# Kernel optimization log

Hardware: AMD Instinct MI355X
Metric: run time of the kernel (lower is better)

Reference implementation:

```python
import jax, jax.numpy as jnp
import numpy as np

B, S, IN = 64, 600, 3
H, C, K = 512, 80, 20
U = 64  # char_len
OUT = 1 + 6 * K


def lstm_cell(x, h, c, W_ih, W_hh, b_ih, b_hh):
    # PyTorch LSTMCell: gates order i, f, g, o
    gates = x @ W_ih.T + b_ih + h @ W_hh.T + b_hh
    i, f, g, o = jnp.split(gates, 4, axis=1)
    i = jax.nn.sigmoid(i)
    f = jax.nn.sigmoid(f)
    g = jnp.tanh(g)
    o = jax.nn.sigmoid(o)
    c_new = f * c + i * g
    h_new = o * jnp.tanh(c_new)
    return h_new, c_new


def setup_inputs() -> dict:
    key = jax.random.key(0)
    ks = jax.random.split(key, 16)
    sc = 0.05
    return {
        "x": jax.random.normal(ks[0], (B, S, IN), jnp.float32),
        "chars": jax.random.uniform(ks[1], (B, U, C), jnp.float32),
        "W_ih1": jax.random.normal(ks[2], (4 * H, IN + C), jnp.float32) * sc,
        "W_hh1": jax.random.normal(ks[3], (4 * H, H), jnp.float32) * sc,
        "b_ih1": jnp.zeros((4 * H,), jnp.float32),
        "b_hh1": jnp.zeros((4 * H,), jnp.float32),
        "W_win": jax.random.normal(ks[4], (3 * K, H), jnp.float32) * sc,
        "b_win": jnp.zeros((3 * K,), jnp.float32),
        "W_ih2": jax.random.normal(ks[5], (4 * H, IN + C), jnp.float32) * sc,
        "W_hh2": jax.random.normal(ks[6], (4 * H, H), jnp.float32) * sc,
        "b_ih2": jnp.zeros((4 * H,), jnp.float32),
        "b_hh2": jnp.zeros((4 * H,), jnp.float32),
        "W_mdn": jax.random.normal(ks[7], (OUT, H), jnp.float32) * sc,
        "b_mdn": jnp.zeros((OUT,), jnp.float32),
    }


def reference(x, chars, W_ih1, W_hh1, b_ih1, b_hh1, W_win, b_win,
              W_ih2, W_hh2, b_ih2, b_hh2, W_mdn, b_mdn):
    u = jnp.arange(U, dtype=x.dtype)[None, None, :]  # [1,1,U]

    def step(carry, pt):
        h1, c1, h2, c2, window, kappa_prev = carry
        inp1 = jnp.concatenate([pt, window], axis=1)           # [B, IN+C]
        h1, c1 = lstm_cell(inp1, h1, c1, W_ih1, W_hh1, b_ih1, b_hh1)
        # Gaussian window attention (Graves)
        wout = h1 @ W_win.T + b_win                            # [B, 3K]
        a, b_, k = jnp.split(wout, 3, axis=1)
        alpha = jnp.exp(a)[:, :, None]                         # [B,K,1]
        beta = jnp.exp(b_)[:, :, None]
        kappa = kappa_prev + jnp.exp(k)                        # [B,K]
        phi = jnp.sum(alpha * jnp.exp(-beta * (kappa[:, :, None] - u) ** 2), axis=1)  # [B,U]
        window = jnp.einsum('bu,buc->bc', phi, chars)          # [B,C]
        inp2 = jnp.concatenate([pt, window], axis=1)
        h2, c2 = lstm_cell(inp2, h2, c2, W_ih2, W_hh2, b_ih2, b_hh2)
        return (h1, c1, h2, c2, window, kappa), h2

    z = jnp.zeros((B, H), x.dtype)
    carry0 = (z, z, z, z, jnp.zeros((B, C), x.dtype), jnp.zeros((B, K), x.dtype))
    _, hs2 = jax.lax.scan(step, carry0, jnp.transpose(x, (1, 0, 2)))  # [S,B,H]
    outputs = jnp.transpose(hs2, (1, 0, 2)).reshape(-1, H)             # [B*S,H]
    mdn = outputs @ W_mdn.T + b_mdn                                     # [B*S,OUT]

    eos = jax.nn.sigmoid(mdn[:, 0]).reshape(-1, 1)
    pi, mu1, mu2, sigma1, sigma2, rho = jnp.split(mdn[:, 1:], 6, axis=1)
    pi = jax.nn.softmax(pi, axis=1)
    sigma1 = jnp.exp(sigma1)
    sigma2 = jnp.exp(sigma2)
    rho = jnp.tanh(rho)
    return eos, pi, mu1, mu2, sigma1, sigma2, rho
```

## Files before the change

### kernel.cpp

```cpp
#include <hip/hip_runtime.h>


typedef unsigned int u32;
typedef unsigned short u16;
typedef unsigned long long u64;
typedef short short8 __attribute__((ext_vector_type(8)));
typedef float floatx4 __attribute__((ext_vector_type(4)));
typedef u32 u32x4 __attribute__((ext_vector_type(4)));

#define NBLK   193
#define NGEMM  128
#define AGG_BID 192
#define NTHR   256
#define SLEN   600

#define OFF_FLAG 0ull
#define OFF_GEN  16384ull
#define OFF_H1P  32768ull
#define OFF_H2P  (OFF_H1P + 131072ull)
#define OFF_WP   (OFF_H2P + 131072ull)
#define OFF_XHI  (OFF_WP + 24576ull)
#define OFF_XLO  (OFF_XHI + 2457600ull)
#define OFF_HS2  (OFF_XLO + 2457600ull)
#define WS_NEED  (OFF_HS2 + 39321600ull)

__device__ __forceinline__ float bf2f(short h) {
  return __uint_as_float(((u32)(u16)h) << 16);
}
__device__ __forceinline__ u16 f2bf(float f) {
  u32 u = __float_as_uint(f);
  u += 0x7fffu + ((u >> 16) & 1u);
  return (u16)(u >> 16);
}
__device__ __forceinline__ float fsig(float x) { return 1.0f / (1.0f + __expf(-x)); }
__device__ __forceinline__ float ftanh_(float x) { return 2.0f / (1.0f + __expf(-2.0f * x)) - 1.0f; }

__device__ __forceinline__ float lstm_point(floatx4 g, float& c) {
  float i  = fsig(g[0]);
  float f  = fsig(g[1]);
  float gg = ftanh_(g[2]);
  float o  = fsig(g[3]);
  c = f * c + i * gg;
  return o * ftanh_(c);
}

__device__ __forceinline__ u32 pack_split(float v) {
  u32 b = __float_as_uint(v);
  float rem = v - __uint_as_float(b & 0xffff0000u);
  return (b >> 16) | ((u32)f2bf(rem) << 16);
}

__device__ __forceinline__ void st_coh(u32* p, u32 v) {
  __hip_atomic_store(p, v, __ATOMIC_RELAXED, __HIP_MEMORY_SCOPE_AGENT);
}
__device__ __forceinline__ u32 ld_coh(const u32* p) {
  return __hip_atomic_load((u32*)p, __ATOMIC_RELAXED, __HIP_MEMORY_SCOPE_AGENT);
}

__device__ __forceinline__ void ld_pk8(const u32* p, short8& hi, short8& lo) {
  u64 d0 = __hip_atomic_load((u64*)(p + 0), __ATOMIC_RELAXED, __HIP_MEMORY_SCOPE_AGENT);
  u64 d1 = __hip_atomic_load((u64*)(p + 2), __ATOMIC_RELAXED, __HIP_MEMORY_SCOPE_AGENT);
  u64 d2 = __hip_atomic_load((u64*)(p + 4), __ATOMIC_RELAXED, __HIP_MEMORY_SCOPE_AGENT);
  u64 d3 = __hip_atomic_load((u64*)(p + 6), __ATOMIC_RELAXED, __HIP_MEMORY_SCOPE_AGENT);
  u32 a0 = (u32)d0, a1 = (u32)(d0 >> 32), a2 = (u32)d1, a3 = (u32)(d1 >> 32);
  u32 a4 = (u32)d2, a5 = (u32)(d2 >> 32), a6 = (u32)d3, a7 = (u32)(d3 >> 32);
  u32x4 h, l;
  h[0] = __builtin_amdgcn_perm(a1, a0, 0x05040100u); l[0] = __builtin_amdgcn_perm(a1, a0, 0x07060302u);
  h[1] = __builtin_amdgcn_perm(a3, a2, 0x05040100u); l[1] = __builtin_amdgcn_perm(a3, a2, 0x07060302u);
  h[2] = __builtin_amdgcn_perm(a5, a4, 0x05040100u); l[2] = __builtin_amdgcn_perm(a5, a4, 0x07060302u);
  h[3] = __builtin_amdgcn_perm(a7, a6, 0x05040100u); l[3] = __builtin_amdgcn_perm(a7, a6, 0x07060302u);
  hi = __builtin_bit_cast(short8, h);
  lo = __builtin_bit_cast(short8, l);
}

__device__ __forceinline__ void sync_wait(u32* flags, u32* gen, u32 lgen, int bid) {
  if (bid == AGG_BID) {
    const int i = threadIdx.x;
    if (i < NBLK) {
      u32 sp = 0;
      while (ld_coh(&flags[i * 16]) < lgen) {
        __builtin_amdgcn_s_sleep(1);
        if (++sp > (1u << 22)) break;
      }
    }
    __syncthreads();
    if (threadIdx.x < 8) st_coh(&gen[threadIdx.x * 16], lgen);
  } else {
    if (threadIdx.x == 0) {
      u32 sp = 0;
      while (ld_coh(&gen[(bid & 7) * 16]) < lgen) {
        __builtin_amdgcn_s_sleep(2);
        if (++sp > (1u << 22)) break;
      }
    }
  }
}

__device__ __forceinline__ void sync_light(u32* flags, u32* gen, u32& lgen, int bid) {
  asm volatile("s_waitcnt vmcnt(0) lgkmcnt(0)" ::: "memory");
  __syncthreads();
  lgen++;
  if (threadIdx.x == 0) st_coh(&flags[bid * 16], lgen);
  sync_wait(flags, gen, lgen, bid);
  __syncthreads();
  asm volatile("" ::: "memory");
}

__device__ __forceinline__ void sync_full(u32* flags, u32* gen, u32& lgen, int bid) {
  __syncthreads();
  lgen++;
  if (threadIdx.x == 0) {
    __threadfence();
    st_coh(&flags[bid * 16], lgen);
  }
  sync_wait(flags, gen, lgen, bid);
  if (threadIdx.x == 0) __threadfence();
  __syncthreads();
  asm volatile("" ::: "memory");
}

__global__ void init_ws(unsigned char* ws) {
  const int gtid = blockIdx.x * 256 + threadIdx.x;
  u32* flg = (u32*)(ws + OFF_FLAG);
  for (int i = gtid; i < NBLK * 16; i += 64 * 256) flg[i] = 0u;
  u32* gn = (u32*)(ws + OFF_GEN);
  if (gtid < 128) gn[gtid] = 0u;
  u32* h2p = (u32*)(ws + OFF_H2P);
  for (int i = gtid; i < 64 * 512; i += 64 * 256) h2p[i] = 0u;
  u32* wp = (u32*)(ws + OFF_WP);
  for (int i = gtid; i < 64 * 96; i += 64 * 256) wp[i] = 0u;
}

__global__ __launch_bounds__(NTHR, 1) void rnn_kernel(
    const float* __restrict__ x, const float* __restrict__ chars,
    const float* __restrict__ Wih1, const float* __restrict__ Whh1,
    const float* __restrict__ bih1, const float* __restrict__ bhh1,
    const float* __restrict__ Wwin, const float* __restrict__ bwin,
    const float* __restrict__ Wih2, const float* __restrict__ Whh2,
    const float* __restrict__ bih2, const float* __restrict__ bhh2,
    const float* __restrict__ Wmdn, const float* __restrict__ bmdn,
    float* __restrict__ out, unsigned char* __restrict__ ws)
{
  const int bid = blockIdx.x;
  const int tid = threadIdx.x;
  const int wid = tid >> 6;
  const int lane = tid & 63;

  u32* flags = (u32*)(ws + OFF_FLAG);
  u32* gen   = (u32*)(ws + OFF_GEN);
  u32* h1p   = (u32*)(ws + OFF_H1P);
  u32* h2p   = (u32*)(ws + OFF_H2P);
  u32* wp    = (u32*)(ws + OFF_WP);
  u16* xhi   = (u16*)(ws + OFF_XHI);
  u16* xlo   = (u16*)(ws + OFF_XLO);
  u16* hs2   = (u16*)(ws + OFF_HS2);

  u32 lgen = 0;

  __shared__ __align__(16) u16 hifrag_s[40 * 512];
  __shared__ __align__(16) u16 lofrag_s[40 * 512];
  __shared__ __align__(16) float chars_s[64 * 80];
  __shared__ __align__(16) float smem_f[512];
  __shared__ float wout_s[64];
  __shared__ float al_s[20], be_s[20], kp_s[20];

  for (int i = bid * NTHR + tid; i < SLEN * 64 * 32; i += NBLK * NTHR) {
    int t = i >> 11;
    int r = i & 2047;
    int bb = r >> 5, q = r & 31;
    float v = (q < 3) ? x[((size_t)bb * SLEN + t) * 3 + q] : 0.0f;
    u32 b = __float_as_uint(v);
    xhi[i] = (u16)(b >> 16);
    xlo[i] = f2bf(v - __uint_as_float(b & 0xffff0000u));
  }

  const bool isg = (bid < NGEMM);
  const bool isw = (bid >= NGEMM && bid < NGEMM + 64);

  float bs1[4], bs2[4];
  float c1 = 0.0f, c2 = 0.0f;
  int b_row = 0, hc = 0;
  float bw = 0.0f;
  const int kg = (lane >> 4) * 8;

  if (isg) {
    b_row = 16 * wid + (lane & 15);
    hc = 4 * bid + (lane >> 4);
    if (wid == 0) {
      const int ra = lane & 15;
      const int origA = (ra & 3) * 512 + 4 * bid + (ra >> 2);
      #pragma unroll
      for (int ks = 0; ks < 20; ++ks) {
        short8 v1h, v1l, v2h, v2l;
        #pragma unroll
        for (int j = 0; j < 8; ++j) {
          int k = 32 * ks + kg + j;
          float a1 = 0.0f, a2 = 0.0f;
          if (k < 512) {
            a1 = Whh1[(size_t)origA * 512 + k];
            a2 = Whh2[(size_t)origA * 512 + k];
          } else if (k < 592) {
            a1 = Wih1[(size_t)origA * 83 + 3 + (k - 512)];
            a2 = Wih2[(size_t)origA * 83 + 3 + (k - 512)];
          } else if (k >= 608 && k < 611) {
            a1 = Wih1[(size_t)origA * 83 + (k - 608)];
            a2 = Wih2[(size_t)origA * 83 + (k - 608)];
          }
          u32 b1 = __float_as_uint(a1), b2 = __float_as_uint(a2);
          v1h[j] = (short)(u16)(b1 >> 16);
          v2h[j] = (short)(u16)(b2 >> 16);
          v1l[j] = (short)f2bf(a1 - __uint_as_float(b1 & 0xffff0000u));
          v2l[j] = (short)f2bf(a2 - __uint_as_float(b2 & 0xffff0000u));
        }
        *(short8*)(hifrag_s + ((0 * 20 + ks) << 9) + (lane << 3)) = v1h;
        *(short8*)(hifrag_s + ((1 * 20 + ks) << 9) + (lane << 3)) = v2h;
        *(short8*)(lofrag_s + ((0 * 20 + ks) << 9) + (lane << 3)) = v1l;
        *(short8*)(lofrag_s + ((1 * 20 + ks) << 9) + (lane << 3)) = v2l;
      }
    }
    #pragma unroll
    for (int r = 0; r < 4; ++r) {
      bs1[r] = bih1[r * 512 + hc] + bhh1[r * 512 + hc];
      bs2[r] = bih2[r * 512 + hc] + bhh2[r * 512 + hc];
    }
  } else if (isw) {
    const int b = bid - NGEMM;
    for (int i = tid; i < 64 * 80; i += NTHR)
      chars_s[i] = chars[(size_t)b * 5120 + i];
    if (tid < 20) kp_s[tid] = 0.0f;
    if (tid < 60) bw = bwin[tid];
  }

  sync_full(flags, gen, lgen, bid);

  if (isg) {
    floatx4 a = { bs1[0], bs1[1], bs1[2], bs1[3] };
    floatx4 b = {0.f,0.f,0.f,0.f}, c = {0.f,0.f,0.f,0.f};
    short8 xh = *(const short8*)(xhi + (size_t)b_row * 32 + kg);
    short8 xl = *(const short8*)(xlo + (size_t)b_row * 32 + kg);
    short8 ah = *(const short8*)(hifrag_s + ((0 * 20 + 19) << 9) + (lane << 3));
    short8 al = *(const short8*)(lofrag_s + ((0 * 20 + 19) << 9) + (lane << 3));
    a = __builtin_amdgcn_mfma_f32_16x16x32_bf16(ah, xh, a, 0, 0, 0);
    b = __builtin_amdgcn_mfma_f32_16x16x32_bf16(ah, xl, b, 0, 0, 0);
    c = __builtin_amdgcn_mfma_f32_16x16x32_bf16(al, xh, c, 0, 0, 0);
    float h = lstm_point(a + b + c, c1);
    st_coh(&h1p[b_row * 512 + hc], pack_split(h));
  }

  sync_light(flags, gen, lgen, bid);

  for (int t = 0; t < SLEN; ++t) {
    floatx4 a1a = {0.f,0.f,0.f,0.f}, a1b = a1a, a1c = a1a;
    floatx4 a2a = {0.f,0.f,0.f,0.f}, a2b = a2a, a2c = a2a;

    if (isg) {
      a2a[0] = bs2[0]; a2a[1] = bs2[1]; a2a[2] = bs2[2]; a2a[3] = bs2[3];
      #pragma unroll
      for (int g = 0; g < 2; ++g) {
        short8 bh[8], bl[8];
        #pragma unroll
        for (int k = 0; k < 8; ++k)
          ld_pk8(h2p + b_row * 512 + (g * 8 + k) * 32 + kg, bh[k], bl[k]);
        #pragma unroll
        for (int k = 0; k < 8; ++k) {
          const int ks = g * 8 + k;
          short8 ah = *(const short8*)(hifrag_s + ((20 + ks) << 9) + (lane << 3));
          short8 al = *(const short8*)(lofrag_s + ((20 + ks) << 9) + (lane << 3));
          a2a = __builtin_amdgcn_mfma_f32_16x16x32_bf16(ah, bh[k], a2a, 0, 0, 0);
          a2b = __builtin_amdgcn_mfma_f32_16x16x32_bf16(ah, bl[k], a2b, 0, 0, 0);
          a2c = __builtin_amdgcn_mfma_f32_16x16x32_bf16(al, bh[k], a2c, 0, 0, 0);
        }
      }
      {
        short8 xh = *(const short8*)(xhi + ((size_t)t * 64 + b_row) * 32 + kg);
        short8 xl = *(const short8*)(xlo + ((size_t)t * 64 + b_row) * 32 + kg);
        short8 ah = *(const short8*)(hifrag_s + ((20 + 19) << 9) + (lane << 3));
        short8 al = *(const short8*)(lofrag_s + ((20 + 19) << 9) + (lane << 3));
        a2a = __builtin_amdgcn_mfma_f32_16x16x32_bf16(ah, xh, a2a, 0, 0, 0);
        a2b = __builtin_amdgcn_mfma_f32_16x16x32_bf16(ah, xl, a2b, 0, 0, 0);
        a2c = __builtin_amdgcn_mfma_f32_16x16x32_bf16(al, xh, a2c, 0, 0, 0);
      }
      if (t < SLEN - 1) {
        a1a[0] = bs1[0]; a1a[1] = bs1[1]; a1a[2] = bs1[2]; a1a[3] = bs1[3];
        #pragma unroll
        for (int g = 0; g < 2; ++g) {
          short8 bh[8], bl[8];
          #pragma unroll
          for (int k = 0; k < 8; ++k)
            ld_pk8(h1p + b_row * 512 + (g * 8 + k) * 32 + kg, bh[k], bl[k]);
          #pragma unroll
          for (int k = 0; k < 8; ++k) {
            const int ks = g * 8 + k;
            short8 ah = *(const short8*)(hifrag_s + (ks << 9) + (lane << 3));
            short8 al = *(const short8*)(lofrag_s + (ks << 9) + (lane << 3));
            a1a = __builtin_amdgcn_mfma_f32_16x16x32_bf16(ah, bh[k], a1a, 0, 0, 0);
            a1b = __builtin_amdgcn_mfma_f32_16x16x32_bf16(ah, bl[k], a1b, 0, 0, 0);
            a1c = __builtin_amdgcn_mfma_f32_16x16x32_bf16(al, bh[k], a1c, 0, 0, 0);
          }
        }
        short8 xh = *(const short8*)(xhi + ((size_t)(t + 1) * 64 + b_row) * 32 + kg);
        short8 xl = *(const short8*)(xlo + ((size_t)(t + 1) * 64 + b_row) * 32 + kg);
        short8 ah = *(const short8*)(hifrag_s + (19 << 9) + (lane << 3));
        short8 al = *(const short8*)(lofrag_s + (19 << 9) + (lane << 3));
        a1a = __builtin_amdgcn_mfma_f32_16x16x32_bf16(ah, xh, a1a, 0, 0, 0);
        a1b = __builtin_amdgcn_mfma_f32_16x16x32_bf16(ah, xl, a1b, 0, 0, 0);
        a1c = __builtin_amdgcn_mfma_f32_16x16x32_bf16(al, xh, a1c, 0, 0, 0);
      }
    } else if (isw) {
      const int b = bid - NGEMM;
      for (int k = tid; k < 512; k += NTHR) {
        u32 p = ld_coh(&h1p[b * 512 + k]);
        smem_f[k] = bf2f((short)(u16)p) + bf2f((short)(u16)(p >> 16));
      }
      __syncthreads();
      const int col = tid & 63;
      const int kq  = tid >> 6;
      float p = 0.0f;
      if (col < 60) {
        const floatx4* wr = (const floatx4*)(Wwin + (size_t)col * 512 + kq * 128);
        const floatx4* hr = (const floatx4*)(smem_f + kq * 128);
        #pragma unroll
        for (int k4 = 0; k4 < 32; ++k4) {
          floatx4 wv = wr[k4];
          floatx4 hv = hr[k4];
          p = fmaf(wv[0], hv[0], p);
          p = fmaf(wv[1], hv[1], p);
          p = fmaf(wv[2], hv[2], p);
          p = fmaf(wv[3], hv[3], p);
        }
      }
      __syncthreads();
      smem_f[tid] = p;
      __syncthreads();
      if (tid < 60)
        wout_s[tid] = smem_f[tid] + smem_f[64 + tid] + smem_f[128 + tid] + smem_f[192 + tid] + bw;
      __syncthreads();
      if (tid < 20) {
        al_s[tid] = __expf(wout_s[tid]);
        be_s[tid] = __expf(wout_s[20 + tid]);
        kp_s[tid] += __expf(wout_s[40 + tid]);
      }
      __syncthreads();
      if (tid < 64) {
        float u = (float)tid;
        float ph = 0.0f;
        #pragma unroll
        for (int k = 0; k < 20; ++k) {
          float d = kp_s[k] - u;
          ph = fmaf(al_s[k], __expf(-be_s[k] * d * d), ph);
        }
        smem_f[256 + tid] = ph;
      }
      __syncthreads();
      if (tid < 80) {
        float wv = 0.0f;
        for (int u = 0; u < 64; ++u)
          wv = fmaf(smem_f[256 + u], chars_s[u * 80 + tid], wv);
        st_coh(&wp[b * 96 + tid], pack_split(wv));
      }
    }

    sync_light(flags, gen, lgen, bid);

    if (isg) {
      short8 wh0, wl0, wh1, wl1, wh2, wl2;
      ld_pk8(wp + b_row * 96 +  0 + kg, wh0, wl0);
      ld_pk8(wp + b_row * 96 + 32 + kg, wh1, wl1);
      ld_pk8(wp + b_row * 96 + 64 + kg, wh2, wl2);
      short8 a2h0 = *(const short8*)(hifrag_s + ((20 + 16) << 9) + (lane << 3));
      short8 a2h1 = *(const short8*)(hifrag_s + ((20 + 17) << 9) + (lane << 3));
      short8 a2h2 = *(const short8*)(hifrag_s + ((20 + 18) << 9) + (lane << 3));
      short8 a2l0 = *(const short8*)(lofrag_s + ((20 + 16) << 9) + (lane << 3));
      short8 a2l1 = *(const short8*)(lofrag_s + ((20 + 17) << 9) + (lane << 3));
      short8 a2l2 = *(const short8*)(lofrag_s + ((20 + 18) << 9) + (lane << 3));
      a2a = __builtin_amdgcn_mfma_f32_16x16x32_bf16(a2h0, wh0, a2a, 0, 0, 0);
      a2b = __builtin_amdgcn_mfma_f32_16x16x32_bf16(a2h0, wl0, a2b, 0, 0, 0);
      a2c = __builtin_amdgcn_mfma_f32_16x16x32_bf16(a2l0, wh0, a2c, 0, 0, 0);
      a2a = __builtin_amdgcn_mfma_f32_16x16x32_bf16(a2h1, wh1, a2a, 0, 0, 0);
      a2b = __builtin_amdgcn_mfma_f32_16x16x32_bf16(a2h1, wl1, a2b, 0, 0, 0);
      a2c = __builtin_amdgcn_mfma_f32_16x16x32_bf16(a2l1, wh1, a2c, 0, 0, 0);
      a2a = __builtin_amdgcn_mfma_f32_16x16x32_bf16(a2h2, wh2, a2a, 0, 0, 0);
      a2b = __builtin_amdgcn_mfma_f32_16x16x32_bf16(a2h2, wl2, a2b, 0, 0, 0);
      a2c = __builtin_amdgcn_mfma_f32_16x16x32_bf16(a2l2, wh2, a2c, 0, 0, 0);
      float h2v = lstm_point(a2a + a2b + a2c, c2);
      st_coh(&h2p[b_row * 512 + hc], pack_split(h2v));
      hs2[((size_t)b_row * SLEN + t) * 512 + hc] = f2bf(h2v);
      if (t < SLEN - 1) {
        short8 a1h0 = *(const short8*)(hifrag_s + (16 << 9) + (lane << 3));
        short8 a1h1 = *(const short8*)(hifrag_s + (17 << 9) + (lane << 3));
        short8 a1h2 = *(const short8*)(hifrag_s + (18 << 9) + (lane << 3));
        short8 a1l0 = *(const short8*)(lofrag_s + (16 << 9) + (lane << 3));
        short8 a1l1 = *(const short8*)(lofrag_s + (17 << 9) + (lane << 3));
        short8 a1l2 = *(const short8*)(lofrag_s + (18 << 9) + (lane << 3));
        a1a = __builtin_amdgcn_mfma_f32_16x16x32_bf16(a1h0, wh0, a1a, 0, 0, 0);
        a1b = __builtin_amdgcn_mfma_f32_16x16x32_bf16(a1h0, wl0, a1b, 0, 0, 0);
        a1c = __builtin_amdgcn_mfma_f32_16x16x32_bf16(a1l0, wh0, a1c, 0, 0, 0);
        a1a = __builtin_amdgcn_mfma_f32_16x16x32_bf16(a1h1, wh1, a1a, 0, 0, 0);
        a1b = __builtin_amdgcn_mfma_f32_16x16x32_bf16(a1h1, wl1, a1b, 0, 0, 0);
        a1c = __builtin_amdgcn_mfma_f32_16x16x32_bf16(a1l1, wh1, a1c, 0, 0, 0);
        a1a = __builtin_amdgcn_mfma_f32_16x16x32_bf16(a1h2, wh2, a1a, 0, 0, 0);
        a1b = __builtin_amdgcn_mfma_f32_16x16x32_bf16(a1h2, wl2, a1b, 0, 0, 0);
        a1c = __builtin_amdgcn_mfma_f32_16x16x32_bf16(a1l2, wh2, a1c, 0, 0, 0);
        float h1v = lstm_point(a1a + a1b + a1c, c1);
        st_coh(&h1p[b_row * 512 + hc], pack_split(h1v));
      }
    }

    sync_light(flags, gen, lgen, bid);
  }

  sync_full(flags, gen, lgen, bid);

  {
    const int row = bid * NTHR + tid;
    if (row < 38400) {
      const u16* hrow = hs2 + (size_t)row * 512;
      {
        float acc = bmdn[0];
        for (int k8 = 0; k8 < 512; k8 += 8) {
          short8 hv = *(const short8*)(hrow + k8);
          #pragma unroll
          for (int j = 0; j < 8; ++j) acc = fmaf(bf2f(hv[j]), Wmdn[k8 + j], acc);
        }
        out[row] = fsig(acc);
      }
      {
        float a[20];
        #pragma unroll
        for (int cc = 0; cc < 20; ++cc) a[cc] = bmdn[1 + cc];
        for (int k8 = 0; k8 < 512; k8 += 8) {
          short8 hv = *(const short8*)(hrow + k8);
          float hf[8];
          #pragma unroll
          for (int j = 0; j < 8; ++j) hf[j] = bf2f(hv[j]);
          #pragma unroll
          for (int cc = 0; cc < 20; ++cc) {
            const float* wr = Wmdn + (size_t)(1 + cc) * 512 + k8;
            #pragma unroll
            for (int j = 0; j < 8; ++j) a[cc] = fmaf(hf[j], wr[j], a[cc]);
          }
        }
        float mx = a[0];
        #pragma unroll
        for (int cc = 1; cc < 20; ++cc) mx = fmaxf(mx, a[cc]);
        float s = 0.0f;
        #pragma unroll
        for (int cc = 0; cc < 20; ++cc) { a[cc] = __expf(a[cc] - mx); s += a[cc]; }
        float inv = 1.0f / s;
        float* po = out + 38400 + (size_t)row * 20;
        #pragma unroll
        for (int cc = 0; cc < 20; ++cc) po[cc] = a[cc] * inv;
      }
      for (int grp = 1; grp <= 5; ++grp) {
        float a[20];
        #pragma unroll
        for (int cc = 0; cc < 20; ++cc) a[cc] = bmdn[1 + 20 * grp + cc];
        for (int k8 = 0; k8 < 512; k8 += 8) {
          short8 hv = *(const short8*)(hrow + k8);
          float hf[8];
          #pragma unroll
          for (int j = 0; j < 8; ++j) hf[j] = bf2f(hv[j]);
          #pragma unroll
          for (int cc = 0; cc < 20; ++cc) {
            const float* wr = Wmdn + (size_t)(1 + 20 * grp + cc) * 512 + k8;
            #pragma unroll
            for (int j = 0; j < 8; ++j) a[cc] = fmaf(hf[j], wr[j], a[cc]);
          }
        }
        float* po = out + 38400 + (size_t)grp * 768000 + (size_t)row * 20;
        if (grp == 3 || grp == 4) {
          #pragma unroll
          for (int cc = 0; cc < 20; ++cc) po[cc] = __expf(a[cc]);
        } else if (grp == 5) {
          #pragma unroll
          for (int cc = 0; cc < 20; ++cc) po[cc] = ftanh_(a[cc]);
        } else {
          #pragma unroll
          for (int cc = 0; cc < 20; ++cc) po[cc] = a[cc];
        }
      }
    }
  }
}

extern "C" void kernel_launch(void* const* d_in, const int* in_sizes, int n_in,
                              void* d_out, int out_size, void* d_ws, size_t ws_size,
                              hipStream_t stream) {
  (void)in_sizes; (void)n_in; (void)out_size;
  if (ws_size < WS_NEED) return;
  init_ws<<<dim3(64), dim3(256), 0, stream>>>((unsigned char*)d_ws);
  rnn_kernel<<<dim3(NBLK), dim3(NTHR), 0, stream>>>(
      (const float*)d_in[0],  (const float*)d_in[1],
      (const float*)d_in[2],  (const float*)d_in[3],
      (const float*)d_in[4],  (const float*)d_in[5],
      (const float*)d_in[6],  (const float*)d_in[7],
      (const float*)d_in[8],  (const float*)d_in[9],
      (const float*)d_in[10], (const float*)d_in[11],
      (const float*)d_in[12], (const float*)d_in[13],
      (float*)d_out, (unsigned char*)d_ws);
}
```

Baseline: 12.86 ms.

## Split recurrent K-reduction across two wave groups per block with LDS partial sums

Doubles the block size to 512 threads and splits each GEMM block's recurrent matmul over the hidden dimension between two 4-wave units. Unit 0 computes the first half of K plus the x input term and writes partial gate sums to shared memory. Unit 1 computes the second half plus the window term, adds the partials and bias, and runs the LSTM pointwise update. The window blocks spread their reduction over 8 waves instead of 4. The aim is to shorten the per-timestep critical path of the serial recurrence, at the cost of extra LDS traffic and more threads per block. It relies on a __syncthreads inside the elided sync code to order the LDS handoff.

```diff
diff --git a/kernel.cpp b/kernel.cpp
--- a/kernel.cpp
+++ b/kernel.cpp
@@ -11,7 +11,7 @@
 #define NBLK   193
 #define NGEMM  128
 #define AGG_BID 192
-#define NTHR   256
+#define NTHR   512
 #define SLEN   600
 
 #define OFF_FLAG 0ull
@@ -145,6 +145,7 @@
   const int tid = threadIdx.x;
   const int wid = tid >> 6;
   const int lane = tid & 63;
+  const int unit = wid >> 2;
 
   u32* flags = (u32*)(ws + OFF_FLAG);
   u32* gen   = (u32*)(ws + OFF_GEN);
@@ -159,6 +160,7 @@
 
   __shared__ __align__(16) u16 hifrag_s[40 * 512];
   __shared__ __align__(16) u16 lofrag_s[40 * 512];
+  __shared__ __align__(16) floatx4 plds[2][256];
   __shared__ __align__(16) float chars_s[64 * 80];
   __shared__ __align__(16) float smem_f[512];
   __shared__ float wout_s[64];
@@ -177,14 +179,14 @@
   const bool isg = (bid < NGEMM);
   const bool isw = (bid >= NGEMM && bid < NGEMM + 64);
 
-  float bs1[4], bs2[4];
+  floatx4 bs1v = {0.f,0.f,0.f,0.f}, bs2v = bs1v;
   float c1 = 0.0f, c2 = 0.0f;
   int b_row = 0, hc = 0;
   float bw = 0.0f;
   const int kg = (lane >> 4) * 8;
 
   if (isg) {
-    b_row = 16 * wid + (lane & 15);
+    b_row = 16 * (wid & 3) + (lane & 15);
     hc = 4 * bid + (lane >> 4);
     if (wid == 0) {
       const int ra = lane & 15;
@@ -220,8 +222,8 @@
     }
     #pragma unroll
     for (int r = 0; r < 4; ++r) {
-      bs1[r] = bih1[r * 512 + hc] + bhh1[r * 512 + hc];
-      bs2[r] = bih2[r * 512 + hc] + bhh2[r * 512 + hc];
+      bs1v[r] = bih1[r * 512 + hc] + bhh1[r * 512 + hc];
+      bs2v[r] = bih2[r * 512 + hc] + bhh2[r * 512 + hc];
     }
   } else if (isw) {
     const int b = bid - NGEMM;
@@ -234,17 +236,23 @@
   sync_full(flags, gen, lgen, bid);
 
   if (isg) {
-    floatx4 a = { bs1[0], bs1[1], bs1[2], bs1[3] };
-    floatx4 b = {0.f,0.f,0.f,0.f}, c = {0.f,0.f,0.f,0.f};
-    short8 xh = *(const short8*)(xhi + (size_t)b_row * 32 + kg);
-    short8 xl = *(const short8*)(xlo + (size_t)b_row * 32 + kg);
-    short8 ah = *(const short8*)(hifrag_s + ((0 * 20 + 19) << 9) + (lane << 3));
-    short8 al = *(const short8*)(lofrag_s + ((0 * 20 + 19) << 9) + (lane << 3));
-    a = __builtin_amdgcn_mfma_f32_16x16x32_bf16(ah, xh, a, 0, 0, 0);
-    b = __builtin_amdgcn_mfma_f32_16x16x32_bf16(ah, xl, b, 0, 0, 0);
-    c = __builtin_amdgcn_mfma_f32_16x16x32_bf16(al, xh, c, 0, 0, 0);
-    float h = lstm_point(a + b + c, c1);
-    st_coh(&h1p[b_row * 512 + hc], pack_split(h));
+    if (unit == 0) {
+      floatx4 a = {0.f,0.f,0.f,0.f}, b = a, c = a;
+      short8 xh = *(const short8*)(xhi + (size_t)b_row * 32 + kg);
+      short8 xl = *(const short8*)(xlo + (size_t)b_row * 32 + kg);
+      short8 ah = *(const short8*)(hifrag_s + (19 << 9) + (lane << 3));
+      short8 al = *(const short8*)(lofrag_s + (19 << 9) + (lane << 3));
+      a = __builtin_amdgcn_mfma_f32_16x16x32_bf16(ah, xh, a, 0, 0, 0);
+      b = __builtin_amdgcn_mfma_f32_16x16x32_bf16(ah, xl, b, 0, 0, 0);
+      c = __builtin_amdgcn_mfma_f32_16x16x32_bf16(al, xh, c, 0, 0, 0);
+      plds[0][tid] = a + b + c;
+    }
+    __syncthreads();
+    if (unit == 1) {
+      floatx4 g = plds[0][tid - 256] + bs1v;
+      float h = lstm_point(g, c1);
+      st_coh(&h1p[b_row * 512 + hc], pack_split(h));
+    }
   }
 
   sync_light(flags, gen, lgen, bid);
@@ -254,73 +262,98 @@
     floatx4 a2a = {0.f,0.f,0.f,0.f}, a2b = a2a, a2c = a2a;
 
     if (isg) {
-      a2a[0] = bs2[0]; a2a[1] = bs2[1]; a2a[2] = bs2[2]; a2a[3] = bs2[3];
-      #pragma unroll
-      for (int g = 0; g < 2; ++g) {
-        short8 bh[8], bl[8];
-        #pragma unroll
-        for (int k = 0; k < 8; ++k)
-          ld_pk8(h2p + b_row * 512 + (g * 8 + k) * 32 + kg, bh[k], bl[k]);
-        #pragma unroll
-        for (int k = 0; k < 8; ++k) {
-          const int ks = g * 8 + k;
-          short8 ah = *(const short8*)(hifrag_s + ((20 + ks) << 9) + (lane << 3));
-          short8 al = *(const short8*)(lofrag_s + ((20 + ks) << 9) + (lane << 3));
-          a2a = __builtin_amdgcn_mfma_f32_16x16x32_bf16(ah, bh[k], a2a, 0, 0, 0);
-          a2b = __builtin_amdgcn_mfma_f32_16x16x32_bf16(ah, bl[k], a2b, 0, 0, 0);
-          a2c = __builtin_amdgcn_mfma_f32_16x16x32_bf16(al, bh[k], a2c, 0, 0, 0);
-        }
-      }
-      {
-        short8 xh = *(const short8*)(xhi + ((size_t)t * 64 + b_row) * 32 + kg);
-        short8 xl = *(const short8*)(xlo + ((size_t)t * 64 + b_row) * 32 + kg);
-        short8 ah = *(const short8*)(hifrag_s + ((20 + 19) << 9) + (lane << 3));
-        short8 al = *(const short8*)(lofrag_s + ((20 + 19) << 9) + (lane << 3));
-        a2a = __builtin_amdgcn_mfma_f32_16x16x32_bf16(ah, xh, a2a, 0, 0, 0);
-        a2b = __builtin_amdgcn_mfma_f32_16x16x32_bf16(ah, xl, a2b, 0, 0, 0);
-        a2c = __builtin_amdgcn_mfma_f32_16x16x32_bf16(al, xh, a2c, 0, 0, 0);
-      }
-      if (t < SLEN - 1) {
-        a1a[0] = bs1[0]; a1a[1] = bs1[1]; a1a[2] = bs1[2]; a1a[3] = bs1[3];
-        #pragma unroll
-        for (int g = 0; g < 2; ++g) {
+      if (unit == 0) {
+        {
+          floatx4 pa = {0.f,0.f,0.f,0.f}, pb = pa, pc = pa;
           short8 bh[8], bl[8];
           #pragma unroll
           for (int k = 0; k < 8; ++k)
-            ld_pk8(h1p + b_row * 512 + (g * 8 + k) * 32 + kg, bh[k], bl[k]);
+            ld_pk8(h2p + b_row * 512 + k * 32 + kg, bh[k], bl[k]);
           #pragma unroll
           for (int k = 0; k < 8; ++k) {
-            const int ks = g * 8 + k;
-            short8 ah = *(const short8*)(hifrag_s + (ks << 9) + (lane << 3));
-            short8 al = *(const short8*)(lofrag_s + (ks << 9) + (lane << 3));
+            short8 ah = *(const short8*)(hifrag_s + ((20 + k) << 9) + (lane << 3));
+            short8 al = *(const short8*)(lofrag_s + ((20 + k) << 9) + (lane << 3));
+            pa = __builtin_amdgcn_mfma_f32_16x16x32_bf16(ah, bh[k], pa, 0, 0, 0);
+            pb = __builtin_amdgcn_mfma_f32_16x16x32_bf16(ah, bl[k], pb, 0, 0, 0);
+            pc = __builtin_amdgcn_mfma_f32_16x16x32_bf16(al, bh[k], pc, 0, 0, 0);
+          }
+          short8 xh = *(const short8*)(xhi + ((size_t)t * 64 + b_row) * 32 + kg);
+          short8 xl = *(const short8*)(xlo + ((size_t)t * 64 + b_row) * 32 + kg);
+          short8 ah = *(const short8*)(hifrag_s + ((20 + 19) << 9) + (lane << 3));
+          short8 al = *(const short8*)(lofrag_s + ((20 + 19) << 9) + (lane << 3));
+          pa = __builtin_amdgcn_mfma_f32_16x16x32_bf16(ah, xh, pa, 0, 0, 0);
+          pb = __builtin_amdgcn_mfma_f32_16x16x32_bf16(ah, xl, pb, 0, 0, 0);
+          pc = __builtin_amdgcn_mfma_f32_16x16x32_bf16(al, xh, pc, 0, 0, 0);
+          plds[1][tid] = pa + pb + pc;
+        }
+        if (t < SLEN - 1) {
+          floatx4 pa = {0.f,0.f,0.f,0.f}, pb = pa, pc = pa;
+          short8 bh[8], bl[8];
+          #pragma unroll
+          for (int k = 0; k < 8; ++k)
+            ld_pk8(h1p + b_row * 512 + k * 32 + kg, bh[k], bl[k]);
+          #pragma unroll
+          for (int k = 0; k < 8; ++k) {
+            short8 ah = *(const short8*)(hifrag_s + (k << 9) + (lane << 3));
+            short8 al = *(const short8*)(lofrag_s + (k << 9) + (lane << 3));
+            pa = __builtin_amdgcn_mfma_f32_16x16x32_bf16(ah, bh[k], pa, 0, 0, 0);
+            pb = __builtin_amdgcn_mfma_f32_16x16x32_bf16(ah, bl[k], pb, 0, 0, 0);
+            pc = __builtin_amdgcn_mfma_f32_16x16x32_bf16(al, bh[k], pc, 0, 0, 0);
+          }
+          short8 xh = *(const short8*)(xhi + ((size_t)(t + 1) * 64 + b_row) * 32 + kg);
+          short8 xl = *(const short8*)(xlo + ((size_t)(t + 1) * 64 + b_row) * 32 + kg);
+          short8 ah = *(const short8*)(hifrag_s + (19 << 9) + (lane << 3));
+          short8 al = *(const short8*)(lofrag_s + (19 << 9) + (lane << 3));
+          pa = __builtin_amdgcn_mfma_f32_16x16x32_bf16(ah, xh, pa, 0, 0, 0);
+          pb = __builtin_amdgcn_mfma_f32_16x16x32_bf16(ah, xl, pb, 0, 0, 0);
+          pc = __builtin_amdgcn_mfma_f32_16x16x32_bf16(al, xh, pc, 0, 0, 0);
+          plds[0][tid] = pa + pb + pc;
+        }
+      } else {
+        {
+          short8 bh[8], bl[8];
+          #pragma unroll
+          for (int k = 0; k < 8; ++k)
+            ld_pk8(h2p + b_row * 512 + (8 + k) * 32 + kg, bh[k], bl[k]);
+          #pragma unroll
+          for (int k = 0; k < 8; ++k) {
+            short8 ah = *(const short8*)(hifrag_s + ((20 + 8 + k) << 9) + (lane << 3));
+            short8 al = *(const short8*)(lofrag_s + ((20 + 8 + k) << 9) + (lane << 3));
+            a2a = __builtin_amdgcn_mfma_f32_16x16x32_bf16(ah, bh[k], a2a, 0, 0, 0);
+            a2b = __builtin_amdgcn_mfma_f32_16x16x32_bf16(ah, bl[k], a2b, 0, 0, 0);
+            a2c = __builtin_amdgcn_mfma_f32_16x16x32_bf16(al, bh[k], a2c, 0, 0, 0);
+          }
+        }
+        if (t < SLEN - 1) {
+          short8 bh[8], bl[8];
+          #pragma unroll
+          for (int k = 0; k < 8; ++k)
+            ld_pk8(h1p + b_row * 512 + (8 + k) * 32 + kg, bh[k], bl[k]);
+          #pragma unroll
+          for (int k = 0; k < 8; ++k) {
+            short8 ah = *(const short8*)(hifrag_s + ((8 + k) << 9) + (lane << 3));
+            short8 al = *(const short8*)(lofrag_s + ((8 + k) << 9) + (lane << 3));
             a1a = __builtin_amdgcn_mfma_f32_16x16x32_bf16(ah, bh[k], a1a, 0, 0, 0);
             a1b = __builtin_amdgcn_mfma_f32_16x16x32_bf16(ah, bl[k], a1b, 0, 0, 0);
             a1c = __builtin_amdgcn_mfma_f32_16x16x32_bf16(al, bh[k], a1c, 0, 0, 0);
           }
         }
-        short8 xh = *(const short8*)(xhi + ((size_t)(t + 1) * 64 + b_row) * 32 + kg);
-        short8 xl = *(const short8*)(xlo + ((size_t)(t + 1) * 64 + b_row) * 32 + kg);
-        short8 ah = *(const short8*)(hifrag_s + (19 << 9) + (lane << 3));
-        short8 al = *(const short8*)(lofrag_s + (19 << 9) + (lane << 3));
-        a1a = __builtin_amdgcn_mfma_f32_16x16x32_bf16(ah, xh, a1a, 0, 0, 0);
-        a1b = __builtin_amdgcn_mfma_f32_16x16x32_bf16(ah, xl, a1b, 0, 0, 0);
-        a1c = __builtin_amdgcn_mfma_f32_16x16x32_bf16(al, xh, a1c, 0, 0, 0);
       }
     } else if (isw) {
       const int b = bid - NGEMM;
-      for (int k = tid; k < 512; k += NTHR) {
-        u32 p = ld_coh(&h1p[b * 512 + k]);
-        smem_f[k] = bf2f((short)(u16)p) + bf2f((short)(u16)(p >> 16));
+      {
+        u32 p = ld_coh(&h1p[b * 512 + tid]);
+        smem_f[tid] = bf2f((short)(u16)p) + bf2f((short)(u16)(p >> 16));
       }
       __syncthreads();
       const int col = tid & 63;
       const int kq  = tid >> 6;
       float p = 0.0f;
       if (col < 60) {
-        const floatx4* wr = (const floatx4*)(Wwin + (size_t)col * 512 + kq * 128);
-        const floatx4* hr = (const floatx4*)(smem_f + kq * 128);
-        #pragma unroll
-        for (int k4 = 0; k4 < 32; ++k4) {
+        const floatx4* wr = (const floatx4*)(Wwin + (size_t)col * 512 + kq * 64);
+        const floatx4* hr = (const floatx4*)(smem_f + kq * 64);
+        #pragma unroll
+        for (int k4 = 0; k4 < 16; ++k4) {
           floatx4 wv = wr[k4];
           floatx4 hv = hr[k4];
           p = fmaf(wv[0], hv[0], p);
@@ -332,8 +365,12 @@
       __syncthreads();
       smem_f[tid] = p;
       __syncthreads();
-      if (tid < 60)
-        wout_s[tid] = smem_f[tid] + smem_f[64 + tid] + smem_f[128 + tid] + smem_f[192 + tid] + bw;
+      if (tid < 60) {
+        float s = 0.0f;
+        #pragma unroll
+        for (int q = 0; q < 8; ++q) s += smem_f[q * 64 + tid];
+        wout_s[tid] = s + bw;
+      }
       __syncthreads();
       if (tid < 20) {
         al_s[tid] = __expf(wout_s[tid]);
@@ -349,59 +386,64 @@
           float d = kp_s[k] - u;
           ph = fmaf(al_s[k], __expf(-be_s[k] * d * d), ph);
         }
-        smem_f[256 + tid] = ph;
+        smem_f[tid] = ph;
       }
       __syncthreads();
       if (tid < 80) {
         float wv = 0.0f;
         for (int u = 0; u < 64; ++u)
-          wv = fmaf(smem_f[256 + u], chars_s[u * 80 + tid], wv);
+          wv = fmaf(smem_f[u], chars_s[u * 80 + tid], wv);
         st_coh(&wp[b * 96 + tid], pack_split(wv));
       }
     }
 
     sync_light(flags, gen, lgen, bid);
 
-    if (isg) {
+    if (isg && unit == 1) {
+      const int j = tid - 256;
       short8 wh0, wl0, wh1, wl1, wh2, wl2;
       ld_pk8(wp + b_row * 96 +  0 + kg, wh0, wl0);
       ld_pk8(wp + b_row * 96 + 32 + kg, wh1, wl1);
       ld_pk8(wp + b_row * 96 + 64 + kg, wh2, wl2);
-      short8 a2h0 = *(const short8*)(hifrag_s + ((20 + 16) << 9) + (lane << 3));
-      short8 a2h1 = *(const short8*)(hifrag_s + ((20 + 17) << 9) + (lane << 3));
-      short8 a2h2 = *(const short8*)(hifrag_s + ((20 + 18) << 9) + (lane << 3));
-      short8 a2l0 = *(const short8*)(lofrag_s + ((20 + 16) << 9) + (lane << 3));
-      short8 a2l1 = *(const short8*)(lofrag_s + ((20 + 17) << 9) + (lane << 3));
-      short8 a2l2 = *(const short8*)(lofrag_s + ((20 + 18) << 9) + (lane << 3));
-      a2a = __builtin_amdgcn_mfma_f32_16x16x32_bf16(a2h0, wh0, a2a, 0, 0, 0);
-      a2b = __builtin_amdgcn_mfma_f32_16x16x32_bf16(a2h0, wl0, a2b, 0, 0, 0);
-      a2c = __builtin_amdgcn_mfma_f32_16x16x32_bf16(a2l0, wh0, a2c, 0, 0, 0);
-      a2a = __builtin_amdgcn_mfma_f32_16x16x32_bf16(a2h1, wh1, a2a, 0, 0, 0);
-      a2b = __builtin_amdgcn_mfma_f32_16x16x32_bf16(a2h1, wl1, a2b, 0, 0, 0);
-      a2c = __builtin_amdgcn_mfma_f32_16x16x32_bf16(a2l1, wh1, a2c, 0, 0, 0);
-      a2a = __builtin_amdgcn_mfma_f32_16x16x32_bf16(a2h2, wh2, a2a, 0, 0, 0);
-      a2b = __builtin_amdgcn_mfma_f32_16x16x32_bf16(a2h2, wl2, a2b, 0, 0, 0);
-      a2c = __builtin_amdgcn_mfma_f32_16x16x32_bf16(a2l2, wh2, a2c, 0, 0, 0);
-      float h2v = lstm_point(a2a + a2b + a2c, c2);
+      {
+        short8 ah0 = *(const short8*)(hifrag_s + ((20 + 16) << 9) + (lane << 3));
+        short8 ah1 = *(const short8*)(hifrag_s + ((20 + 17) << 9) + (lane << 3));
+        short8 ah2 = *(const short8*)(hifrag_s + ((20 + 18) << 9) + (lane << 3));
+        short8 al0 = *(const short8*)(lofrag_s + ((20 + 16) << 9) + (lane << 3));
+        short8 al1 = *(const short8*)(lofrag_s + ((20 + 17) << 9) + (lane << 3));
+        short8 al2 = *(const short8*)(lofrag_s + ((20 + 18) << 9) + (lane << 3));
+        a2a = __builtin_amdgcn_mfma_f32_16x16x32_bf16(ah0, wh0, a2a, 0, 0, 0);
+        a2b = __builtin_amdgcn_mfma_f32_16x16x32_bf16(ah0, wl0, a2b, 0, 0, 0);
+        a2c = __builtin_amdgcn_mfma_f32_16x16x32_bf16(al0, wh0, a2c, 0, 0, 0);
+        a2a = __builtin_amdgcn_mfma_f32_16x16x32_bf16(ah1, wh1, a2a, 0, 0, 0);
+        a2b = __builtin_amdgcn_mfma_f32_16x16x32_bf16(ah1, wl1, a2b, 0, 0, 0);
+        a2c = __builtin_amdgcn_mfma_f32_16x16x32_bf16(al1, wh1, a2c, 0, 0, 0);
+        a2a = __builtin_amdgcn_mfma_f32_16x16x32_bf16(ah2, wh2, a2a, 0, 0, 0);
+        a2b = __builtin_amdgcn_mfma_f32_16x16x32_bf16(ah2, wl2, a2b, 0, 0, 0);
+        a2c = __builtin_amdgcn_mfma_f32_16x16x32_bf16(al2, wh2, a2c, 0, 0, 0);
+      }
+      floatx4 g2 = a2a + a2b + a2c + plds[1][j] + bs2v;
+      float h2v = lstm_point(g2, c2);
       st_coh(&h2p[b_row * 512 + hc], pack_split(h2v));
       hs2[((size_t)b_row * SLEN + t) * 512 + hc] = f2bf(h2v);
       if (t < SLEN - 1) {
-        short8 a1h0 = *(const short8*)(hifrag_s + (16 << 9) + (lane << 3));
-        short8 a1h1 = *(const short8*)(hifrag_s + (17 << 9) + (lane << 3));
-        short8 a1h2 = *(const short8*)(hifrag_s + (18 << 9) + (lane << 3));
-        short8 a1l0 = *(const short8*)(lofrag_s + (16 << 9) + (lane << 3));
-        short8 a1l1 = *(const short8*)(lofrag_s + (17 << 9) + (lane << 3));
-        short8 a1l2 = *(const short8*)(lofrag_s + (18 << 9) + (lane << 3));
-        a1a = __builtin_amdgcn_mfma_f32_16x16x32_bf16(a1h0, wh0, a1a, 0, 0, 0);
-        a1b = __builtin_amdgcn_mfma_f32_16x16x32_bf16(a1h0, wl0, a1b, 0, 0, 0);
-        a1c = __builtin_amdgcn_mfma_f32_16x16x32_bf16(a1l0, wh0, a1c, 0, 0, 0);
-        a1a = __builtin_amdgcn_mfma_f32_16x16x32_bf16(a1h1, wh1, a1a, 0, 0, 0);
-        a1b = __builtin_amdgcn_mfma_f32_16x16x32_bf16(a1h1, wl1, a1b, 0, 0, 0);
-        a1c = __builtin_amdgcn_mfma_f32_16x16x32_bf16(a1l1, wh1, a1c, 0, 0, 0);
-        a1a = __builtin_amdgcn_mfma_f32_16x16x32_bf16(a1h2, wh2, a1a, 0, 0, 0);
-        a1b = __builtin_amdgcn_mfma_f32_16x16x32_bf16(a1h2, wl2, a1b, 0, 0, 0);
-        a1c = __builtin_amdgcn_mfma_f32_16x16x32_bf16(a1l2, wh2, a1c, 0, 0, 0);
-        float h1v = lstm_point(a1a + a1b + a1c, c1);
+        short8 ah0 = *(const short8*)(hifrag_s + (16 << 9) + (lane << 3));
+        short8 ah1 = *(const short8*)(hifrag_s + (17 << 9) + (lane << 3));
+        short8 ah2 = *(const short8*)(hifrag_s + (18 << 9) + (lane << 3));
+        short8 al0 = *(const short8*)(lofrag_s + (16 << 9) + (lane << 3));
+        short8 al1 = *(const short8*)(lofrag_s + (17 << 9) + (lane << 3));
+        short8 al2 = *(const short8*)(lofrag_s + (18 << 9) + (lane << 3));
+        a1a = __builtin_amdgcn_mfma_f32_16x16x32_bf16(ah0, wh0, a1a, 0, 0, 0);
+        a1b = __builtin_amdgcn_mfma_f32_16x16x32_bf16(ah0, wl0, a1b, 0, 0, 0);
+        a1c = __builtin_amdgcn_mfma_f32_16x16x32_bf16(al0, wh0, a1c, 0, 0, 0);
+        a1a = __builtin_amdgcn_mfma_f32_16x16x32_bf16(ah1, wh1, a1a, 0, 0, 0);
+        a1b = __builtin_amdgcn_mfma_f32_16x16x32_bf16(ah1, wl1, a1b, 0, 0, 0);
+        a1c = __builtin_amdgcn_mfma_f32_16x16x32_bf16(al1, wh1, a1c, 0, 0, 0);
+        a1a = __builtin_amdgcn_mfma_f32_16x16x32_bf16(ah2, wh2, a1a, 0, 0, 0);
+        a1b = __builtin_amdgcn_mfma_f32_16x16x32_bf16(ah2, wl2, a1b, 0, 0, 0);
+        a1c = __builtin_amdgcn_mfma_f32_16x16x32_bf16(al2, wh2, a1c, 0, 0, 0);
+        floatx4 g1 = a1a + a1b + a1c + plds[0][j] + bs1v;
+        float h1v = lstm_point(g1, c1);
         st_coh(&h1p[b_row * 512 + hc], pack_split(h1v));
       }
     }
```

Result: faster. 12.31 ms (-4.3%).
